# Optimization experiments

Measured on AMD Instinct MI355X. Metric: run time of the kernel, lower is better.

The kernel has to match this reference:

```python
import jax, jax.numpy as jnp
import numpy as np

B, N, D, DA = 8, 2048, 512, 64


def setup_inputs() -> dict:
    key = jax.random.key(0)
    ks = jax.random.split(key, 10)
    s = 1.0 / np.sqrt(D)
    return {
        "x": jax.random.normal(ks[0], (B, N, D), jnp.float32),
        "query_aux": jax.random.normal(ks[1], (B, N, DA), jnp.float32),
        "key_aux": jax.random.normal(ks[2], (B, N, DA), jnp.float32),
        "adjacency_mask": jax.random.randint(ks[3], (B, N, N), 0, 2, jnp.int32),
        "merge_coefficients": jax.random.uniform(ks[4], (1,), jnp.float32),
        "Wq": jax.random.normal(ks[5], (D, D), jnp.float32) * s,
        "bq": jnp.zeros((D,), jnp.float32),
        "Wk": jax.random.normal(ks[6], (D, D), jnp.float32) * s,
        "bk": jnp.zeros((D,), jnp.float32),
        "Wv": jax.random.normal(ks[7], (D, D), jnp.float32) * s,
        "bv": jnp.zeros((D,), jnp.float32),
        "threshold": jnp.float32(0.5),
    }


def reference(x, query_aux, key_aux, adjacency_mask, merge_coefficients,
              Wq, bq, Wk, bk, Wv, bv, threshold):
    d_model = Wq.shape[0]
    scale = jnp.asarray(d_model, x.dtype) ** 0.5
    # torch nn.Linear: y = x @ W.T + b
    q = jnp.einsum('bnd,ed->bne', x, Wq) + bq
    k = jnp.einsum('bnd,ed->bne', x, Wk) + bk
    v = jnp.einsum('bnd,ed->bne', x, Wv) + bv

    scores = jnp.einsum('bne,bme->bnm', q, k) / scale  # [B,N,N]

    aux_scale = jnp.asarray(key_aux.shape[-1], x.dtype) ** 0.5
    scores_aux = jnp.einsum('bna,bma->bnm', query_aux, key_aux) / aux_scale

    merge_mask = (scores_aux != 0) & (scores > threshold)
    c = merge_coefficients
    merged = (1.0 - c) * scores + c * scores_aux
    scores = jnp.where(merge_mask, merged, scores)

    mask_value = jnp.finfo(scores.dtype).min
    scores = jnp.where(adjacency_mask == 0, mask_value, scores)

    weights = jax.nn.softmax(scores, axis=-1)
    return jnp.einsum('bnm,bme->bne', weights, v)
```

## Files before the change

### kernel.cpp

```cpp
#include <hip/hip_runtime.h>
#include <cstdint>

typedef _Float16 f16;
typedef _Float16 f16x4 __attribute__((ext_vector_type(4)));
typedef _Float16 f16x8 __attribute__((ext_vector_type(8)));
typedef float    f32x4 __attribute__((ext_vector_type(4)));

#define MFMA(a,b,c) __builtin_amdgcn_mfma_f32_16x16x32_f16((a),(b),(c),0,0,0)

constexpr int  Bb = 8, Nn = 2048, Dd = 512, Ad = 64;
constexpr long XN = (long)Bb*Nn*Dd;
constexpr long WN = (long)Dd*Dd;
constexpr long AN = (long)Bb*Nn*Ad;
constexpr float LO_S  = 4096.f;
constexpr float LO_INV= 1.f/4096.f;
constexpr float P_SC  = 1024.f;
constexpr float NEGF  = -3.402823466e38f;

#define KSWZ(row, cb2) ((row)*256  + ((cb2) ^ (((row)&7)<<4)))
#define QSWZ(row, cb2) ((row)*1024 + ((cb2) ^ (((row)&7)<<4)))

__device__ __forceinline__ void gload16(const void* g, void* l) {
  __builtin_amdgcn_global_load_lds(
      (const __attribute__((address_space(1))) void*)g,
      (__attribute__((address_space(3))) void*)l, 16, 0, 0);
}

__global__ void prep_split(const float* __restrict__ x,
  const float* __restrict__ Wq, const float* __restrict__ Wk, const float* __restrict__ Wv,
  const float* __restrict__ aq, const float* __restrict__ ak,
  f16* __restrict__ xh, f16* __restrict__ xl, f16* __restrict__ Wh, f16* __restrict__ Wl,
  f16* __restrict__ aqh, f16* __restrict__ akh)
{
  const long total4 = (XN + 3*WN + 2*AN) >> 2;
  for (long u = blockIdx.x*(long)blockDim.x + threadIdx.x; u < total4;
       u += (long)gridDim.x*blockDim.x) {
    long i = u << 2;
    if (i < XN) {
      float4 v = *(const float4*)(x + i);
      float vv[4] = {v.x, v.y, v.z, v.w};
      f16x4 h, l;
      #pragma unroll
      for (int t=0;t<4;++t){ f16 hh=(f16)vv[t]; h[t]=hh; l[t]=(f16)((vv[t]-(float)hh)*LO_S); }
      *(f16x4*)(xh+i)=h; *(f16x4*)(xl+i)=l;
    } else if (i < XN + 3*WN) {
      long j = i - XN;
      const float* w = (j < WN) ? (Wq + j) : (j < 2*WN ? (Wk + (j-WN)) : (Wv + (j-2*WN)));
      float4 v = *(const float4*)w;
      float vv[4] = {v.x, v.y, v.z, v.w};
      f16x4 h, l;
      #pragma unroll
      for (int t=0;t<4;++t){ f16 hh=(f16)vv[t]; h[t]=hh; l[t]=(f16)((vv[t]-(float)hh)*LO_S); }
      *(f16x4*)(Wh+j)=h; *(f16x4*)(Wl+j)=l;
    } else {
      long j = i - XN - 3*WN;
      const float* s = (j < AN) ? (aq + j) : (ak + (j-AN));
      f16*         d = (j < AN) ? (aqh + j) : (akh + (j-AN));
      float4 v = *(const float4*)s;
      float vv[4] = {v.x, v.y, v.z, v.w};
      f16x4 h;
      #pragma unroll
      for (int t=0;t<4;++t) h[t]=(f16)vv[t];
      *(f16x4*)d = h;
    }
  }
}

__global__ __launch_bounds__(256, 2) void proj_qk(
  const f16* __restrict__ xh, const f16* __restrict__ xl,
  const f16* __restrict__ Wh, const f16* __restrict__ Wl,
  const float* __restrict__ bq, const float* __restrict__ bk,
  f16* __restrict__ qh, f16* __restrict__ ql,
  f16* __restrict__ kh, f16* __restrict__ kl)
{
  const int z = blockIdx.z;
  const f16* Whz = Wh + (long)z*WN;
  const f16* Wlz = Wl + (long)z*WN;
  const float* bias = z ? bk : bq;
  f16* oh = z ? kh : qh;
  f16* ol = z ? kl : ql;
  const int e0 = blockIdx.x*128, m0 = blockIdx.y*128;
  __shared__ f16 Ah[128][40], Al[128][40], Bh[128][40], Bl[128][40];
  const int tid = threadIdx.x, lane = tid & 63, wid = tid >> 6;
  const int wi = wid & 1, wj = wid >> 1;
  const int r16 = lane & 15, g16 = lane >> 4;

  f32x4 acch[4][4], accl[4][4];
  #pragma unroll
  for (int a=0;a<4;++a)
    #pragma unroll
    for (int bI=0;bI<4;++bI){ acch[a][bI]=(f32x4){0.f,0.f,0.f,0.f}; accl[a][bI]=(f32x4){0.f,0.f,0.f,0.f}; }

  f16x8 st[8];
  #pragma unroll
  for (int t=0;t<2;++t) {
    int u = tid + t*256; int row = u>>2, sg = u&3;
    long ko = (long)sg*8;
    st[t*4+0] = *(const f16x8*)&Whz[(long)(e0+row)*Dd + ko];
    st[t*4+1] = *(const f16x8*)&Wlz[(long)(e0+row)*Dd + ko];
    st[t*4+2] = *(const f16x8*)&xh [(long)(m0+row)*Dd + ko];
    st[t*4+3] = *(const f16x8*)&xl [(long)(m0+row)*Dd + ko];
  }
  for (int kt=0; kt<16; ++kt) {
    __syncthreads();
    #pragma unroll
    for (int t=0;t<2;++t) {
      int u = tid + t*256; int row = u>>2, sg = u&3;
      *(f16x8*)&Ah[row][sg*8] = st[t*4+0];
      *(f16x8*)&Al[row][sg*8] = st[t*4+1];
      *(f16x8*)&Bh[row][sg*8] = st[t*4+2];
      *(f16x8*)&Bl[row][sg*8] = st[t*4+3];
    }
    __syncthreads();
    if (kt < 15) {
      #pragma unroll
      for (int t=0;t<2;++t) {
        int u = tid + t*256; int row = u>>2, sg = u&3;
        long ko = (long)(kt+1)*32 + sg*8;
        st[t*4+0] = *(const f16x8*)&Whz[(long)(e0+row)*Dd + ko];
        st[t*4+1] = *(const f16x8*)&Wlz[(long)(e0+row)*Dd + ko];
        st[t*4+2] = *(const f16x8*)&xh [(long)(m0+row)*Dd + ko];
        st[t*4+3] = *(const f16x8*)&xl [(long)(m0+row)*Dd + ko];
      }
    }
    f16x8 ahf[4], alf[4];
    #pragma unroll
    for (int fi=0;fi<4;++fi) {
      ahf[fi] = *(const f16x8*)&Ah[wi*64 + fi*16 + r16][g16*8];
      alf[fi] = *(const f16x8*)&Al[wi*64 + fi*16 + r16][g16*8];
    }
    #pragma unroll
    for (int fj=0;fj<4;++fj) {
      f16x8 bhf = *(const f16x8*)&Bh[wj*64 + fj*16 + r16][g16*8];
      f16x8 blf = *(const f16x8*)&Bl[wj*64 + fj*16 + r16][g16*8];
      #pragma unroll
      for (int fi=0;fi<4;++fi) {
        acch[fi][fj] = MFMA(ahf[fi], bhf, acch[fi][fj]);
        accl[fi][fj] = MFMA(ahf[fi], blf, accl[fi][fj]);
        accl[fi][fj] = MFMA(alf[fi], bhf, accl[fi][fj]);
      }
    }
  }
  #pragma unroll
  for (int fi=0;fi<4;++fi) {
    const int eb = e0 + wi*64 + fi*16 + g16*4;
    const float4 b4 = *(const float4*)&bias[eb];
    const float bbv[4] = {b4.x, b4.y, b4.z, b4.w};
    #pragma unroll
    for (int fj=0;fj<4;++fj) {
      const int xr = m0 + wj*64 + fj*16 + r16;
      f16x4 h4, l4;
      #pragma unroll
      for (int rg=0;rg<4;++rg) {
        float v = acch[fi][fj][rg] + accl[fi][fj][rg]*LO_INV + bbv[rg];
        f16 hh = (f16)v;
        h4[rg] = hh;
        l4[rg] = (f16)((v - (float)hh)*LO_S);
      }
      *(f16x4*)&oh[(long)xr*Dd + eb] = h4;
      *(f16x4*)&ol[(long)xr*Dd + eb] = l4;
    }
  }
}

__global__ __launch_bounds__(256, 2) void proj_v(
  const f16* __restrict__ xh, const f16* __restrict__ Wvh,
  const float* __restrict__ bv, f16* __restrict__ vT)
{
  const int e0 = blockIdx.x*128, m0 = blockIdx.y*128;
  __shared__ f16 Ax[128][40], Bw[128][40];
  const int tid = threadIdx.x, lane = tid & 63, wid = tid >> 6;
  const int wi = wid & 1, wj = wid >> 1;
  const int r16 = lane & 15, g16 = lane >> 4;

  f32x4 acc[4][4];
  #pragma unroll
  for (int a=0;a<4;++a)
    #pragma unroll
    for (int bI=0;bI<4;++bI) acc[a][bI]=(f32x4){0.f,0.f,0.f,0.f};

  f16x8 st[4];
  #pragma unroll
  for (int t=0;t<2;++t) {
    int u = tid + t*256; int row = u>>2, sg = u&3;
    st[t*2+0] = *(const f16x8*)&xh [(long)(m0+row)*Dd + sg*8];
    st[t*2+1] = *(const f16x8*)&Wvh[(long)(e0+row)*Dd + sg*8];
  }
  for (int kt=0; kt<16; ++kt) {
    __syncthreads();
    #pragma unroll
    for (int t=0;t<2;++t) {
      int u = tid + t*256; int row = u>>2, sg = u&3;
      *(f16x8*)&Ax[row][sg*8] = st[t*2+0];
      *(f16x8*)&Bw[row][sg*8] = st[t*2+1];
    }
    __syncthreads();
    if (kt < 15) {
      #pragma unroll
      for (int t=0;t<2;++t) {
        int u = tid + t*256; int row = u>>2, sg = u&3;
        long ko = (long)(kt+1)*32 + sg*8;
        st[t*2+0] = *(const f16x8*)&xh [(long)(m0+row)*Dd + ko];
        st[t*2+1] = *(const f16x8*)&Wvh[(long)(e0+row)*Dd + ko];
      }
    }
    f16x8 af[4];
    #pragma unroll
    for (int fi=0;fi<4;++fi) af[fi] = *(const f16x8*)&Ax[wi*64 + fi*16 + r16][g16*8];
    #pragma unroll
    for (int fj=0;fj<4;++fj) {
      f16x8 bf = *(const f16x8*)&Bw[wj*64 + fj*16 + r16][g16*8];
      #pragma unroll
      for (int fi=0;fi<4;++fi) acc[fi][fj] = MFMA(af[fi], bf, acc[fi][fj]);
    }
  }
  #pragma unroll
  for (int fj=0;fj<4;++fj) {
    const int e = e0 + wj*64 + fj*16 + r16;
    const float bve = bv[e];
    #pragma unroll
    for (int fi=0;fi<4;++fi) {
      const int xr0 = m0 + wi*64 + fi*16 + g16*4;
      const int bbi = xr0 >> 11, nn = xr0 & 2047;
      f16x4 h4;
      #pragma unroll
      for (int rg=0;rg<4;++rg) h4[rg] = (f16)(acc[fi][fj][rg] + bve);
      *(f16x4*)&vT[((long)bbi*Dd + e)*Nn + nn] = h4;
    }
  }
}

constexpr int FLASH_LDS = 151552;

__global__ __launch_bounds__(512) void flash(
  const f16* __restrict__ qhg, const f16* __restrict__ qlg,
  const f16* __restrict__ khg, const f16* __restrict__ klg,
  const f16* __restrict__ vT,  const f16* __restrict__ aqg, const f16* __restrict__ akg,
  const int* __restrict__ adj, const float* __restrict__ mcp, const float* __restrict__ thp,
  float* __restrict__ out)
{
  extern __shared__ char smem[];
  char* QLb  = smem;
  char* KHb0 = smem + 65536;
  char* KHb1 = smem + 81920;
  char* KLb0 = smem + 98304;
  char* KLb1 = smem + 114688;
  f16 (* __restrict__ AK)[72] = (f16(*)[72])(smem + 131072);
  f16 (* __restrict__ PS)[72] = (f16(*)[72])(smem + 140288);
  float* pmax = (float*)(smem + 149504);
  float* psum = pmax + 128;
  float* mnew = psum + 128;
  float* scl  = mnew + 64;
  float* mst  = scl + 64;
  float* lst  = mst + 64;

  const int b  = blockIdx.y;
  const int r0 = blockIdx.x * 64;
  const int tid = threadIdx.x;
  const int lane = tid & 63, wid = tid >> 6;
  const int wm = wid & 3, wn = wid >> 2;
  const int r16 = lane & 15, g16 = lane >> 4;
  const int g16c = g16 * 16;
  const int qrow = wm*16 + r16;
  const float cc = mcp[0], thr = thp[0];

  if (tid < 64) { mst[tid] = NEGF; lst[tid] = 0.f; }

  const long qbase = ((long)(b*Nn + r0))*Dd;
  for (int u = tid; u < 4096; u += 512) {
    int row = u >> 6, sg = u & 63;
    *(f16x8*)(QLb + QSWZ(row, sg*16)) = *(const f16x8*)&qlg[qbase + (long)row*Dd + sg*8];
  }
  f16x8 qhr[16];
  {
    const f16* qrp = qhg + qbase + (long)qrow*Dd;
    #pragma unroll
    for (int ks=0; ks<16; ++ks) qhr[ks] = *(const f16x8*)&qrp[ks*32 + g16*8];
  }
  f16x8 aqr[2];
  {
    const f16* arow = aqg + ((long)(b*Nn + r0 + qrow))*Ad;
    aqr[0] = *(const f16x8*)&arow[g16*8];
    aqr[1] = *(const f16x8*)&arow[32 + g16*8];
  }
  f32x4 oacc[4][4];
  #pragma unroll
  for (int i=0;i<4;++i)
    #pragma unroll
    for (int j=0;j<4;++j) oacc[i][j] = (f32x4){0.f,0.f,0.f,0.f};

  const int srow = (lane >> 4);
  const int schunkbase = lane & 15;

  {
    const long gb = ((long)(b*Nn))*Dd;
    #pragma unroll
    for (int t=0; t<2; ++t) {
      const int row = wid*8 + t*4 + srow;
      const int gch = schunkbase ^ (t*4 + srow);
      const long go = gb + (long)row*Dd + gch*8;
      gload16(khg + go, KHb0 + wid*2048 + t*1024);
      gload16(klg + go, KLb0 + wid*2048 + t*1024);
    }
  }
  __syncthreads();

  for (int ct=0; ct<Nn/64; ++ct) {
    const int cb = ct*64;
    f32x4 sacc[2], slo[2], aacc[2];
    #pragma unroll
    for (int nf=0;nf<2;++nf){ sacc[nf]=(f32x4){0.f,0.f,0.f,0.f}; slo[nf]=(f32x4){0.f,0.f,0.f,0.f}; aacc[nf]=(f32x4){0.f,0.f,0.f,0.f}; }

    for (int kc=0; kc<4; ++kc) {
      const int slot = ct*4 + kc;
      char* KHc = (slot & 1) ? KHb1 : KHb0;
      char* KLc = (slot & 1) ? KLb1 : KLb0;
      if (slot < 127) {
        const int ns = slot + 1;
        char* KHn = (ns & 1) ? KHb1 : KHb0;
        char* KLn = (ns & 1) ? KLb1 : KLb0;
        const long gb = ((long)(b*Nn + (ns>>2)*64))*Dd + (ns&3)*128;
        #pragma unroll
        for (int t=0; t<2; ++t) {
          const int row = wid*8 + t*4 + srow;
          const int gch = schunkbase ^ (t*4 + srow);
          const long go = gb + (long)row*Dd + gch*8;
          gload16(khg + go, KHn + wid*2048 + t*1024);
          gload16(klg + go, KLn + wid*2048 + t*1024);
        }
      }
      f16x8 sak;
      if (kc == 2)
        sak = *(const f16x8*)&akg[((long)(b*Nn + cb))*Ad + (long)(tid>>3)*Ad + (tid&7)*8];

      #pragma unroll
      for (int k4=0; k4<4; ++k4) {
        const int ks = kc*4 + k4;
        f16x8 alo = *(const f16x8*)(QLb + QSWZ(qrow, ks*64 + g16c));
        #pragma unroll
        for (int nf=0; nf<2; ++nf) {
          const int cr = wn*32 + nf*16 + r16;
          f16x8 bh = *(const f16x8*)(KHc + KSWZ(cr, k4*64 + g16c));
          f16x8 bl = *(const f16x8*)(KLc + KSWZ(cr, k4*64 + g16c));
          sacc[nf] = MFMA(qhr[ks], bh, sacc[nf]);
          slo[nf]  = MFMA(qhr[ks], bl, slo[nf]);
          slo[nf]  = MFMA(alo,     bh, slo[nf]);
        }
      }
      if (kc == 2) *(f16x8*)&AK[tid>>3][(tid&7)*8] = sak;
      __syncthreads();
    }
    int adjv[2][4];
    {
      const int* ap = adj + ((long)(b*Nn + r0 + wm*16))*Nn + cb + wn*32 + r16;
      #pragma unroll
      for (int nf=0; nf<2; ++nf)
        #pragma unroll
        for (int rg=0; rg<4; ++rg)
          adjv[nf][rg] = ap[(long)(g16*4+rg)*Nn + nf*16];
    }
    #pragma unroll
    for (int ks=0; ks<2; ++ks)
      #pragma unroll
      for (int nf=0; nf<2; ++nf) {
        f16x8 bf = *(const f16x8*)&AK[wn*32 + nf*16 + r16][ks*32 + g16*8];
        aacc[nf] = MFMA(aqr[ks], bf, aacc[nf]);
      }
    float sv[2][4], mx[4];
    #pragma unroll
    for (int rg=0; rg<4; ++rg) {
      #pragma unroll
      for (int nf=0; nf<2; ++nf) {
        float s = (sacc[nf][rg] + slo[nf][rg]*LO_INV) / 22.627416997969522f;
        float a = aacc[nf][rg] * 0.125f;
        float m = (1.f - cc)*s + cc*a;
        s = ((a != 0.f) && (s > thr)) ? m : s;
        sv[nf][rg] = adjv[nf][rg] ? s : NEGF;
      }
      mx[rg] = fmaxf(sv[0][rg], sv[1][rg]);
    }
    #pragma unroll
    for (int off=1; off<16; off<<=1)
      #pragma unroll
      for (int rg=0; rg<4; ++rg)
        mx[rg] = fmaxf(mx[rg], __shfl_xor(mx[rg], off));
    if (r16 == 0) {
      #pragma unroll
      for (int rg=0; rg<4; ++rg) pmax[wn*64 + wm*16 + g16*4 + rg] = mx[rg];
    }
    __syncthreads();
    if (tid < 64) {
      float tmax = fmaxf(pmax[tid], pmax[64+tid]);
      float mo = mst[tid];
      float mn = fmaxf(mo, tmax);
      mnew[tid] = mn;
      scl[tid]  = __expf(mo - mn);
      mst[tid]  = mn;
    }
    __syncthreads();
    float sm[4];
    #pragma unroll
    for (int rg=0; rg<4; ++rg) {
      const int rr = wm*16 + g16*4 + rg;
      const float mn = mnew[rr];
      float p0 = __expf(sv[0][rg] - mn);
      float p1 = __expf(sv[1][rg] - mn);
      PS[rr][wn*32 + r16]      = (f16)(p0 * P_SC);
      PS[rr][wn*32 + 16 + r16] = (f16)(p1 * P_SC);
      sm[rg] = p0 + p1;
    }
    #pragma unroll
    for (int off=1; off<16; off<<=1)
      #pragma unroll
      for (int rg=0; rg<4; ++rg)
        sm[rg] += __shfl_xor(sm[rg], off);
    if (r16 == 0) {
      #pragma unroll
      for (int rg=0; rg<4; ++rg) psum[wn*64 + wm*16 + g16*4 + rg] = sm[rg];
    }
    __syncthreads();
    if (tid < 64) lst[tid] = lst[tid]*scl[tid] + psum[tid] + psum[64+tid];
    float scj[4];
    #pragma unroll
    for (int j=0;j<4;++j) scj[j] = scl[j*16 + r16];
    #pragma unroll
    for (int i=0;i<4;++i)
      #pragma unroll
      for (int j=0;j<4;++j)
        #pragma unroll
        for (int rg=0;rg<4;++rg) oacc[i][j][rg] *= scj[j];
    #pragma unroll
    for (int ks=0; ks<2; ++ks) {
      f16x8 va[4];
      const f16* vb = vT + ((long)(b*Dd) + wid*64 + r16)*Nn + cb + ks*32 + g16*8;
      #pragma unroll
      for (int i=0;i<4;++i) va[i] = *(const f16x8*)&vb[(long)i*16*Nn];
      #pragma unroll
      for (int j=0;j<4;++j) {
        f16x8 pb = *(const f16x8*)&PS[j*16 + r16][ks*32 + g16*8];
        #pragma unroll
        for (int i=0;i<4;++i) oacc[i][j] = MFMA(va[i], pb, oacc[i][j]);
      }
    }
  }
  __syncthreads();
  const long ob = ((long)(b*Nn + r0))*Dd;
  #pragma unroll
  for (int j=0;j<4;++j) {
    const int rr = j*16 + r16;
    const float li = 1.f / (lst[rr] * P_SC);
    #pragma unroll
    for (int i=0;i<4;++i) {
      f32x4 v;
      #pragma unroll
      for (int rg=0;rg<4;++rg) v[rg] = oacc[i][j][rg] * li;
      *(f32x4*)&out[ob + (long)rr*Dd + wid*64 + i*16 + g16*4] = v;
    }
  }
}

extern "C" void kernel_launch(void* const* d_in, const int* in_sizes, int n_in,
                              void* d_out, int out_size, void* d_ws, size_t ws_size,
                              hipStream_t stream)
{
  const float* x   = (const float*)d_in[0];
  const float* qa  = (const float*)d_in[1];
  const float* ka  = (const float*)d_in[2];
  const int*   adj = (const int*)  d_in[3];
  const float* mc  = (const float*)d_in[4];
  const float* Wq  = (const float*)d_in[5];
  const float* bq  = (const float*)d_in[6];
  const float* Wk  = (const float*)d_in[7];
  const float* bk  = (const float*)d_in[8];
  const float* Wv  = (const float*)d_in[9];
  const float* bv  = (const float*)d_in[10];
  const float* th  = (const float*)d_in[11];
  float* out = (float*)d_out;

  f16* p  = (f16*)d_ws;
  f16* xh = p;  p += XN;
  f16* xl = p;  p += XN;
  f16* Wh = p;  p += 3*WN;
  f16* Wl = p;  p += 3*WN;
  f16* qh = p;  p += XN;
  f16* ql = p;  p += XN;
  f16* kh = p;  p += XN;
  f16* kl = p;  p += XN;
  f16* vT = p;  p += XN;
  f16* aqh = p; p += AN;
  f16* akh = p; p += AN;

  prep_split<<<dim3(2048), dim3(256), 0, stream>>>(x, Wq, Wk, Wv, qa, ka,
                                                   xh, xl, Wh, Wl, aqh, akh);
  proj_qk<<<dim3(4,128,2), dim3(256), 0, stream>>>(xh, xl, Wh, Wl, bq, bk,
                                                   qh, ql, kh, kl);
  proj_v<<<dim3(4,128), dim3(256), 0, stream>>>(xh, Wh + 2*WN, bv, vT);

  hipFuncSetAttribute(reinterpret_cast<const void*>(flash),
                      hipFuncAttributeMaxDynamicSharedMemorySize, FLASH_LDS);
  flash<<<dim3(Nn/64, Bb), dim3(512), FLASH_LDS, stream>>>(qh, ql, kh, kl, vT,
                                                           aqh, akh, adj, mc, th, out);
}
```

Baseline: 452.3 us.

## Stream Q-high fragments per chunk, drop AK LDS staging, remove a softmax barrier

Replaces the 16-register Q-high fragment array with two 4-entry buffers reloaded from global memory each k-chunk, which cuts register pressure. The aux-key tile is now read straight from global memory instead of being staged through LDS, and the per-row max/scale bookkeeping is folded into the exp pass so one __syncthreads per tile goes away. In exchange, Q-high is re-fetched from global/L2 on every column tile, and there is a possible race: mst/sclA are written while other waves may still be reading mst before the next barrier.

Result: slower. 562.8 us (+24.4%).

```diff
diff --git a/kernel.cpp b/kernel.cpp
--- a/kernel.cpp
+++ b/kernel.cpp
@@ -230,7 +230,7 @@
   }
 }
 
-constexpr int FLASH_LDS = 151552;
+constexpr int FLASH_LDS = 142080;
 
 __global__ __launch_bounds__(512) void flash(
   const f16* __restrict__ qhg, const f16* __restrict__ qlg,
@@ -245,14 +245,12 @@
   char* KHb1 = smem + 81920;
   char* KLb0 = smem + 98304;
   char* KLb1 = smem + 114688;
-  f16 (* __restrict__ AK)[72] = (f16(*)[72])(smem + 131072);
-  f16 (* __restrict__ PS)[72] = (f16(*)[72])(smem + 140288);
-  float* pmax = (float*)(smem + 149504);
+  f16 (* __restrict__ PS)[72] = (f16(*)[72])(smem + 131072);
+  float* pmax = (float*)(smem + 140288);
   float* psum = pmax + 128;
-  float* mnew = psum + 128;
-  float* scl  = mnew + 64;
-  float* mst  = scl + 64;
+  float* mst  = psum + 128;
   float* lst  = mst + 64;
+  float* sclA = lst + 64;
 
   const int b  = blockIdx.y;
   const int r0 = blockIdx.x * 64;
@@ -271,12 +269,10 @@
     int row = u >> 6, sg = u & 63;
     *(f16x8*)(QLb + QSWZ(row, sg*16)) = *(const f16x8*)&qlg[qbase + (long)row*Dd + sg*8];
   }
-  f16x8 qhr[16];
-  {
-    const f16* qrp = qhg + qbase + (long)qrow*Dd;
-    #pragma unroll
-    for (int ks=0; ks<16; ++ks) qhr[ks] = *(const f16x8*)&qrp[ks*32 + g16*8];
-  }
+  const f16* qrp = qhg + qbase + (long)qrow*Dd + g16*8;
+  f16x8 qA[4], qB[4];
+  #pragma unroll
+  for (int t=0;t<4;++t) qA[t] = *(const f16x8*)&qrp[t*32];
   f16x8 aqr[2];
   {
     const f16* arow = aqg + ((long)(b*Nn + r0 + qrow))*Ad;
@@ -311,6 +307,7 @@
     #pragma unroll
     for (int nf=0;nf<2;++nf){ sacc[nf]=(f32x4){0.f,0.f,0.f,0.f}; slo[nf]=(f32x4){0.f,0.f,0.f,0.f}; aacc[nf]=(f32x4){0.f,0.f,0.f,0.f}; }
 
+    #pragma unroll
     for (int kc=0; kc<4; ++kc) {
       const int slot = ct*4 + kc;
       char* KHc = (slot & 1) ? KHb1 : KHb0;
@@ -329,10 +326,13 @@
           gload16(klg + go, KLn + wid*2048 + t*1024);
         }
       }
-      f16x8 sak;
-      if (kc == 2)
-        sak = *(const f16x8*)&akg[((long)(b*Nn + cb))*Ad + (long)(tid>>3)*Ad + (tid&7)*8];
-
+      {
+        const int nk = (kc+1)&3;
+        f16x8* qn = (kc&1) ? qA : qB;
+        #pragma unroll
+        for (int t=0;t<4;++t) qn[t] = *(const f16x8*)&qrp[(nk*4+t)*32];
+      }
+      const f16x8* qc = (kc&1) ? qB : qA;
       #pragma unroll
       for (int k4=0; k4<4; ++k4) {
         const int ks = kc*4 + k4;
@@ -342,12 +342,11 @@
           const int cr = wn*32 + nf*16 + r16;
           f16x8 bh = *(const f16x8*)(KHc + KSWZ(cr, k4*64 + g16c));
           f16x8 bl = *(const f16x8*)(KLc + KSWZ(cr, k4*64 + g16c));
-          sacc[nf] = MFMA(qhr[ks], bh, sacc[nf]);
-          slo[nf]  = MFMA(qhr[ks], bl, slo[nf]);
-          slo[nf]  = MFMA(alo,     bh, slo[nf]);
+          sacc[nf] = MFMA(qc[k4], bh, sacc[nf]);
+          slo[nf]  = MFMA(qc[k4], bl, slo[nf]);
+          slo[nf]  = MFMA(alo,    bh, slo[nf]);
         }
       }
-      if (kc == 2) *(f16x8*)&AK[tid>>3][(tid&7)*8] = sak;
       __syncthreads();
     }
     int adjv[2][4];
@@ -363,7 +362,7 @@
     for (int ks=0; ks<2; ++ks)
       #pragma unroll
       for (int nf=0; nf<2; ++nf) {
-        f16x8 bf = *(const f16x8*)&AK[wn*32 + nf*16 + r16][ks*32 + g16*8];
+        const f16x8 bf = *(const f16x8*)&akg[((long)(b*Nn + cb + wn*32 + nf*16 + r16))*Ad + ks*32 + g16*8];
         aacc[nf] = MFMA(aqr[ks], bf, aacc[nf]);
       }
     float sv[2][4], mx[4];
@@ -389,25 +388,22 @@
       for (int rg=0; rg<4; ++rg) pmax[wn*64 + wm*16 + g16*4 + rg] = mx[rg];
     }
     __syncthreads();
-    if (tid < 64) {
-      float tmax = fmaxf(pmax[tid], pmax[64+tid]);
-      float mo = mst[tid];
-      float mn = fmaxf(mo, tmax);
-      mnew[tid] = mn;
-      scl[tid]  = __expf(mo - mn);
-      mst[tid]  = mn;
-    }
-    __syncthreads();
     float sm[4];
     #pragma unroll
     for (int rg=0; rg<4; ++rg) {
       const int rr = wm*16 + g16*4 + rg;
-      const float mn = mnew[rr];
+      const float tm = fmaxf(pmax[rr], pmax[64+rr]);
+      const float mo = mst[rr];
+      const float mn = fmaxf(mo, tm);
       float p0 = __expf(sv[0][rg] - mn);
       float p1 = __expf(sv[1][rg] - mn);
       PS[rr][wn*32 + r16]      = (f16)(p0 * P_SC);
       PS[rr][wn*32 + 16 + r16] = (f16)(p1 * P_SC);
       sm[rg] = p0 + p1;
+      if (r16 == 0 && wn == 0) {
+        sclA[rr] = __expf(mo - mn);
+        mst[rr]  = mn;
+      }
     }
     #pragma unroll
     for (int off=1; off<16; off<<=1)
@@ -419,10 +415,16 @@
       for (int rg=0; rg<4; ++rg) psum[wn*64 + wm*16 + g16*4 + rg] = sm[rg];
     }
     __syncthreads();
-    if (tid < 64) lst[tid] = lst[tid]*scl[tid] + psum[tid] + psum[64+tid];
+    if (r16 == 0 && wn == 0) {
+      #pragma unroll
+      for (int rg=0; rg<4; ++rg) {
+        const int rr = wm*16 + g16*4 + rg;
+        lst[rr] = lst[rr]*sclA[rr] + psum[rr] + psum[64+rr];
+      }
+    }
     float scj[4];
     #pragma unroll
-    for (int j=0;j<4;++j) scj[j] = scl[j*16 + r16];
+    for (int j=0;j<4;++j) scj[j] = sclA[j*16 + r16];
     #pragma unroll
     for (int i=0;i<4;++i)
       #pragma unroll
```
